# Optimization experiments

Hardware: AMD Instinct MI355X
Metric: run time of the kernel (lower is better)

Reference implementation:

```python
import jax, jax.numpy as jnp
import numpy as np

D_MODEL = 512
EPS = 1e-5  # torch LayerNorm default


def _layernorm(x, g, b):
    mu = jnp.mean(x, axis=-1, keepdims=True)
    var = jnp.mean(jnp.square(x - mu), axis=-1, keepdims=True)
    return (x - mu) * jax.lax.rsqrt(var + EPS) * g + b


def setup_inputs() -> dict:
    key = jax.random.key(0)
    ks = jax.random.split(key, 12)
    d = D_MODEL
    s = 1.0 / np.sqrt(d)
    s4 = 1.0 / np.sqrt(4 * d)
    return {
        "x": jax.random.normal(ks[0], (4, 4096, d), dtype=jnp.float32),
        "Wq": jax.random.uniform(ks[1], (d, d), jnp.float32, -s, s),
        "bq": jax.random.uniform(ks[2], (d,), jnp.float32, -s, s),
        "Wk": jax.random.uniform(ks[3], (d, d), jnp.float32, -s, s),
        "bk": jax.random.uniform(ks[4], (d,), jnp.float32, -s, s),
        "Wv": jax.random.uniform(ks[5], (d, d), jnp.float32, -s, s),
        "bv": jax.random.uniform(ks[6], (d,), jnp.float32, -s, s),
        "g1": jnp.ones((d,), jnp.float32),
        "b1": jnp.zeros((d,), jnp.float32),
        "g2": jnp.ones((d,), jnp.float32),
        "b2": jnp.zeros((d,), jnp.float32),
        "W1": jax.random.uniform(ks[7], (d, 4 * d), jnp.float32, -s, s),
        "bf1": jax.random.uniform(ks[8], (4 * d,), jnp.float32, -s, s),
        "W2": jax.random.uniform(ks[9], (4 * d, d), jnp.float32, -s4, s4),
        "bf2": jax.random.uniform(ks[10], (d,), jnp.float32, -s4, s4),
    }


def reference(x, Wq, bq, Wk, bk, Wv, bv, g1, b1, g2, b2, W1, bf1, W2, bf2):
    # QKV projections: [b, s, d]
    Q = jnp.einsum("bsd,de->bse", x, Wq) + bq
    K = jnp.einsum("bsd,de->bse", x, Wk) + bk
    V = jnp.einsum("bsd,de->bse", x, Wv) + bv
    scale = 1.0 / jnp.sqrt(jnp.float32(K.shape[-1]))
    scores = jnp.einsum("bqd,bkd->bqk", Q, K) * scale  # [b, s, s]
    attn = jax.nn.softmax(scores, axis=-1)
    att = jnp.einsum("bqk,bkd->bqd", attn, V)
    x = _layernorm(x + att, g1, b1)
    h = jax.nn.relu(jnp.einsum("bsd,df->bsf", x, W1) + bf1)
    ffn = jnp.einsum("bsf,fd->bsd", h, W2) + bf2
    return _layernorm(x + ffn, g2, b2)
```

## Files before the change

kernel.cpp:

```cpp
#include <hip/hip_runtime.h>
#include <hip/hip_bf16.h>

typedef unsigned short u16;
typedef short bf16x8 __attribute__((ext_vector_type(8)));
typedef float f32x4 __attribute__((ext_vector_type(4)));

__device__ __forceinline__ float b2f(u16 u) {
  union { float f; unsigned int i; } v; v.i = ((unsigned int)u) << 16; return v.f;
}
__device__ __forceinline__ u16 f2b(float f) {
  union { float f; unsigned int i; } v; v.f = f;
  unsigned int r = v.i + 0x7fffu + ((v.i >> 16) & 1u);
  return (u16)(r >> 16);
}
__device__ __forceinline__ u16 to_b(float v) { return f2b(v); }
__device__ __forceinline__ u16 to_b(u16 v) { return v; }

__device__ __forceinline__ void gl_lds16(const u16* g, u16* l) {
  __builtin_amdgcn_global_load_lds(
      (const __attribute__((address_space(1))) unsigned int*)g,
      (__attribute__((address_space(3))) unsigned int*)l, 16, 0, 0);
}

#define VMW4()  asm volatile("s_waitcnt vmcnt(4)" ::: "memory")
#define VMW0()  asm volatile("s_waitcnt vmcnt(0)" ::: "memory")
#define CFENCE() asm volatile("" ::: "memory")

template <bool RELU, bool ATOMIC>
__global__ __launch_bounds__(256)
void gemm_nt(const u16* __restrict__ A, const u16* __restrict__ Bt,
             const float* __restrict__ bias, void* __restrict__ Cv,
             int N, int K, int nsplit, int lda, int ldb, int ldc,
             long sA, long sB, long sC, float scale) {
  __shared__ __align__(16) u16 As[128 * 64];
  __shared__ __align__(16) u16 Bs[128 * 64];
  const int z = blockIdx.z;
  const int batch = z / nsplit, split = z - batch * nsplit;
  const int Ks = K / nsplit;
  const u16* Ab = A + (long)batch * sA + (long)split * Ks;
  const u16* Bb = Bt + (long)batch * sB + (long)split * Ks;
  const int f = blockIdx.x + gridDim.x * blockIdx.y;
  const int xcd = f & 7, idx = f >> 3;
  const int bx = idx % gridDim.x;
  const int by = xcd * (gridDim.y >> 3) + idx / gridDim.x;
  const int m0 = by * 128, n0 = bx * 128;
  const int t = threadIdx.x, w = t >> 6, lane = t & 63;
  const int wm = (w >> 1) * 64, wn = (w & 1) * 64;
  const int lr = lane & 15, q = lane >> 4;

  int srow[4], scol[4];
#pragma unroll
  for (int i = 0; i < 4; i++) {
    int n = w * 256 + i * 64 + lane;
    srow[i] = n >> 3;
    scol[i] = (((n & 7) ^ ((n >> 3) & 7)) * 8);
  }

  f32x4 acc[4][4];
#pragma unroll
  for (int i = 0; i < 4; i++)
#pragma unroll
    for (int j = 0; j < 4; j++) acc[i][j] = (f32x4){0.f, 0.f, 0.f, 0.f};

  for (int k0 = 0; k0 < Ks; k0 += 64) {
#pragma unroll
    for (int i = 0; i < 4; i++)
      gl_lds16(Ab + (long)(m0 + srow[i]) * lda + k0 + scol[i], &As[(w * 256 + i * 64) * 8]);
#pragma unroll
    for (int i = 0; i < 4; i++)
      gl_lds16(Bb + (long)(n0 + srow[i]) * ldb + k0 + scol[i], &Bs[(w * 256 + i * 64) * 8]);
    __syncthreads();
#pragma unroll
    for (int kk = 0; kk < 2; kk++) {
      bf16x8 af[4], bfr[4];
#pragma unroll
      for (int i = 0; i < 4; i++) {
        int row = wm + i * 16 + lr;
        af[i] = *(const bf16x8*)&As[row * 64 + (((kk * 4 + q) ^ (row & 7)) * 8)];
      }
#pragma unroll
      for (int j = 0; j < 4; j++) {
        int row = wn + j * 16 + lr;
        bfr[j] = *(const bf16x8*)&Bs[row * 64 + (((kk * 4 + q) ^ (row & 7)) * 8)];
      }
#pragma unroll
      for (int i = 0; i < 4; i++)
#pragma unroll
        for (int j = 0; j < 4; j++)
          acc[i][j] = __builtin_amdgcn_mfma_f32_16x16x32_bf16(af[i], bfr[j], acc[i][j], 0, 0, 0);
    }
    __syncthreads();
  }

#pragma unroll
  for (int j = 0; j < 4; j++) {
    int cg = n0 + wn + j * 16 + lr;
    float bb = (!ATOMIC && bias) ? bias[cg] : 0.0f;
#pragma unroll
    for (int i = 0; i < 4; i++) {
      int rbase = m0 + wm + i * 16 + q * 4;
#pragma unroll
      for (int r = 0; r < 4; r++) {
        float vv = acc[i][j][r] * scale;
        if (ATOMIC) {
          atomicAdd((float*)Cv + (long)batch * sC + (long)(rbase + r) * ldc + cg, vv);
        } else {
          vv += bb;
          if (RELU) vv = fmaxf(vv, 0.0f);
          ((u16*)Cv)[(long)batch * sC + (long)(rbase + r) * ldc + cg] = f2b(vv);
        }
      }
    }
  }
}

#define STAGE_K(kvv, kcc, sel)                                               \
  {                                                                          \
    _Pragma("unroll") for (int rr = 0; rr < 4; rr++)                         \
        gl_lds16(Kbase + (long)((kvv) * 128 + srow[rr]) * 1536 +             \
                     (kcc) * 128 + scol8[rr],                                \
                 &B2[(sel)][ldsd[rr]]);                                      \
  }
#define STAGE_V(kvv, dcc, sel)                                               \
  {                                                                          \
    _Pragma("unroll") for (int rr = 0; rr < 4; rr++)                         \
        gl_lds16(Vtb + (long)((dcc) * 128 + srow[rr]) * 4096 +               \
                     (kvv) * 128 + scol8[rr],                                \
                 &B2[(sel)][ldsd[rr]]);                                      \
  }

__global__ __launch_bounds__(512, 2)
void flash_attn(const u16* __restrict__ QKV, const u16* __restrict__ Vt,
                u16* __restrict__ attp, float* __restrict__ lbp, float scl) {
  __shared__ __align__(16) u16 B2[2][128 * 128];
  __shared__ __align__(16) u16 Pb[128 * 136];
  const int flat = blockIdx.x;
  const int batch = (flat & 7) >> 1, half = flat & 1, qt = flat >> 3;
  const int t = threadIdx.x, w = t >> 6, lane = t & 63;
  const int lr = lane & 15, q = lane >> 4;
  const long rowbase = (long)batch * 4096 + qt * 128;
  const u16* Qrow  = QKV + (rowbase + w * 16 + lr) * 1536;
  const u16* Kbase = QKV + ((long)batch * 4096 + half * 2048) * 1536 + 512;
  const u16* Vtb   = Vt + (long)batch * 512 * 4096 + half * 2048;
  u16* Pw = &Pb[w * (16 * 136)];

  int srow[4], scol8[4], ldsd[4];
#pragma unroll
  for (int rr = 0; rr < 4; rr++) {
    int n = rr * 512 + t;
    srow[rr] = n >> 4;
    scol8[rr] = ((n & 15) ^ ((n >> 4) & 15)) * 8;
    ldsd[rr] = (rr * 512 + w * 64) * 8;
  }

  f32x4 O[32];
#pragma unroll
  for (int i = 0; i < 32; i++) O[i] = (f32x4){0.f, 0.f, 0.f, 0.f};
  float lsum[4] = {0.f, 0.f, 0.f, 0.f};

  STAGE_K(0, 0, 0);
  int par = 0;

  for (int kv = 0; kv < 16; kv++) {
    f32x4 S[8];
#pragma unroll
    for (int j = 0; j < 8; j++) S[j] = (f32x4){0.f, 0.f, 0.f, 0.f};

#pragma unroll
    for (int kc = 0; kc < 4; kc++) {
      bf16x8 Qf[4];
#pragma unroll
      for (int ss = 0; ss < 4; ss++)
        Qf[ss] = *(const bf16x8*)(Qrow + kc * 128 + ss * 32 + q * 8);
      __builtin_amdgcn_sched_barrier(0);
      if (kc < 3) { STAGE_K(kv, kc + 1, par ^ 1); }
      else        { STAGE_V(kv, 0, par ^ 1); }
      VMW4();
      __builtin_amdgcn_s_barrier();
      CFENCE();
      __builtin_amdgcn_s_setprio(1);
#pragma unroll
      for (int ss = 0; ss < 4; ss++)
#pragma unroll
        for (int j = 0; j < 8; j++) {
          int row = j * 16 + lr;
          bf16x8 Kf = *(const bf16x8*)&B2[par][row * 128 + (((ss * 4 + q) ^ lr) * 8)];
          S[j] = __builtin_amdgcn_mfma_f32_16x16x32_bf16(Qf[ss], Kf, S[j], 0, 0, 0);
        }
      __builtin_amdgcn_s_setprio(0);
      CFENCE();
      __builtin_amdgcn_s_barrier();
      par ^= 1;
    }

    float psum[4] = {0.f, 0.f, 0.f, 0.f};
#pragma unroll
    for (int j = 0; j < 8; j++)
#pragma unroll
      for (int r = 0; r < 4; r++) {
        float e = __expf(S[j][r] * scl);
        psum[r] += e;
        Pw[(q * 4 + r) * 136 + j * 16 + lr] = f2b(e);
      }
#pragma unroll
    for (int r = 0; r < 4; r++) {
#pragma unroll
      for (int o = 1; o < 16; o <<= 1) psum[r] += __shfl_xor(psum[r], o);
      lsum[r] += psum[r];
    }
    bf16x8 Pf[4];
#pragma unroll
    for (int t4 = 0; t4 < 4; t4++)
      Pf[t4] = *(const bf16x8*)&Pw[lr * 136 + t4 * 32 + q * 8];

#pragma unroll
    for (int dc = 0; dc < 4; dc++) {
      if (dc < 3) {
        STAGE_V(kv, dc + 1, par ^ 1);
        VMW4();
      } else if (kv < 15) {
        STAGE_K(kv + 1, 0, par ^ 1);
        VMW4();
      } else {
        VMW0();
      }
      __builtin_amdgcn_s_barrier();
      CFENCE();
      __builtin_amdgcn_s_setprio(1);
#pragma unroll
      for (int t4 = 0; t4 < 4; t4++)
#pragma unroll
        for (int j = 0; j < 8; j++) {
          int row = j * 16 + lr;
          bf16x8 Vf = *(const bf16x8*)&B2[par][row * 128 + (((t4 * 4 + q) ^ lr) * 8)];
          O[dc * 8 + j] = __builtin_amdgcn_mfma_f32_16x16x32_bf16(Pf[t4], Vf, O[dc * 8 + j], 0, 0, 0);
        }
      __builtin_amdgcn_s_setprio(0);
      CFENCE();
      __builtin_amdgcn_s_barrier();
      par ^= 1;
    }
  }

  u16* op = attp + (long)half * 16384 * 512;
#pragma unroll
  for (int i = 0; i < 32; i++) {
    int col = (i >> 3) * 128 + (i & 7) * 16 + lr;
#pragma unroll
    for (int r = 0; r < 4; r++)
      op[(rowbase + w * 16 + q * 4 + r) * 512 + col] = f2b(O[i][r]);
  }
  if (lr == 0)
#pragma unroll
    for (int r = 0; r < 4; r++)
      lbp[(long)half * 16384 + rowbase + w * 16 + q * 4 + r] = lsum[r];
}

template <typename TS>
__global__ __launch_bounds__(1024)
void transpose_b(const TS* __restrict__ src, u16* __restrict__ dst,
                 int R, int Cc, int src_ld, long sbs, long dbs) {
  __shared__ u16 tile[32][33];
  int r = blockIdx.y * 32 + threadIdx.y;
  int c = blockIdx.x * 32 + threadIdx.x;
  tile[threadIdx.y][threadIdx.x] = to_b(src[(long)blockIdx.z * sbs + (long)r * src_ld + c]);
  __syncthreads();
  int rr = blockIdx.x * 32 + threadIdx.y;
  int cc = blockIdx.y * 32 + threadIdx.x;
  dst[(long)blockIdx.z * dbs + (long)rr * R + cc] = tile[threadIdx.x][threadIdx.y];
}

__global__ __launch_bounds__(1024)
void prep(const float* __restrict__ Wq, const float* __restrict__ Wk,
          const float* __restrict__ Wv, const float* __restrict__ W1,
          const float* __restrict__ W2, const float* __restrict__ bq,
          const float* __restrict__ bk, const float* __restrict__ bv,
          const float* __restrict__ x, u16* __restrict__ wqkvt,
          u16* __restrict__ w1t, u16* __restrict__ w2t,
          float* __restrict__ bqkv, u16* __restrict__ xb) {
  __shared__ u16 tile[32][33];
  const int b = blockIdx.x;
  const int t = threadIdx.x;
  const int tx = t & 31, ty = t >> 5;
  if (b < 768) {
    const int wsel = b >> 8, idx = b & 255;
    const int bx = idx & 15, by = idx >> 4;
    const float* src = wsel == 0 ? Wq : (wsel == 1 ? Wk : Wv);
    u16* dst = wqkvt + wsel * 512 * 512;
    tile[ty][tx] = f2b(src[(by * 32 + ty) * 512 + bx * 32 + tx]);
    __syncthreads();
    dst[(bx * 32 + ty) * 512 + by * 32 + tx] = tile[tx][ty];
  } else if (b < 1792) {
    const int idx = b - 768;
    const int bx = idx & 63, by = idx >> 6;
    tile[ty][tx] = f2b(W1[(by * 32 + ty) * 2048 + bx * 32 + tx]);
    __syncthreads();
    w1t[(bx * 32 + ty) * 512 + by * 32 + tx] = tile[tx][ty];
  } else if (b < 2816) {
    const int idx = b - 1792;
    const int bx = idx & 15, by = idx >> 4;
    tile[ty][tx] = f2b(W2[(by * 32 + ty) * 512 + bx * 32 + tx]);
    __syncthreads();
    w2t[(bx * 32 + ty) * 2048 + by * 32 + tx] = tile[tx][ty];
  } else if (b < 3840) {
    const long i = ((long)(b - 2816) * 1024 + t) * 8;
    float4 a0 = *(const float4*)(x + i);
    float4 a1 = *(const float4*)(x + i + 4);
    u16 tmp[8] = {f2b(a0.x), f2b(a0.y), f2b(a0.z), f2b(a0.w),
                  f2b(a1.x), f2b(a1.y), f2b(a1.z), f2b(a1.w)};
    *(uint4*)(xb + i) = *(uint4*)tmp;
  } else {
    const int i = (b - 3840) * 1024 + t;
    if (i < 512) bqkv[i] = bq[i];
    else if (i < 1024) bqkv[i] = bk[i - 512];
    else if (i < 1536) bqkv[i] = bv[i - 1024];
  }
}

__global__ __launch_bounds__(256)
void add_ln_att(const float* __restrict__ X, const u16* __restrict__ attp,
                const float* __restrict__ lbp,
                const float* __restrict__ g, const float* __restrict__ b,
                u16* __restrict__ O) {
  const int row = blockIdx.x * 4 + (threadIdx.x >> 6);
  const int lane = threadIdx.x & 63;
  const size_t base = (size_t)row * 512 + lane * 8;
  const float inv = 1.0f / (lbp[row] + lbp[16384 + row]);
  uint4 p0 = *(const uint4*)(attp + base);
  uint4 p1 = *(const uint4*)(attp + 16384L * 512 + base);
  const u16* s0 = (const u16*)&p0;
  const u16* s1 = (const u16*)&p1;
  float z[8];
  float s1a = 0.f, s2a = 0.f;
#pragma unroll
  for (int i = 0; i < 8; i++) {
    z[i] = X[base + i] + (b2f(s0[i]) + b2f(s1[i])) * inv;
    s1a += z[i]; s2a += z[i] * z[i];
  }
#pragma unroll
  for (int o = 32; o > 0; o >>= 1) { s1a += __shfl_xor(s1a, o); s2a += __shfl_xor(s2a, o); }
  const float mu = s1a * (1.0f / 512.0f);
  const float var = s2a * (1.0f / 512.0f) - mu * mu;
  const float rstd = rsqrtf(var + 1e-5f);
#pragma unroll
  for (int i = 0; i < 8; i++) {
    int c = lane * 8 + i;
    O[base + i] = f2b((z[i] - mu) * rstd * g[c] + b[c]);
  }
}

__global__ __launch_bounds__(256)
void add_ln_ffn(const u16* __restrict__ X, const u16* __restrict__ P0,
                const u16* __restrict__ P1, const float* __restrict__ eb,
                const float* __restrict__ g, const float* __restrict__ b,
                float* __restrict__ O) {
  const int row = blockIdx.x * 4 + (threadIdx.x >> 6);
  const int lane = threadIdx.x & 63;
  const size_t base = (size_t)row * 512 + lane * 8;
  uint4 xv = *(const uint4*)(X + base);
  uint4 a0 = *(const uint4*)(P0 + base);
  uint4 a1 = *(const uint4*)(P1 + base);
  const u16* xs = (const u16*)&xv;
  const u16* s0 = (const u16*)&a0;
  const u16* s1 = (const u16*)&a1;
  float z[8];
  float s1a = 0.f, s2a = 0.f;
#pragma unroll
  for (int i = 0; i < 8; i++) {
    int c = lane * 8 + i;
    z[i] = b2f(xs[i]) + b2f(s0[i]) + b2f(s1[i]) + eb[c];
    s1a += z[i]; s2a += z[i] * z[i];
  }
#pragma unroll
  for (int o = 32; o > 0; o >>= 1) { s1a += __shfl_xor(s1a, o); s2a += __shfl_xor(s2a, o); }
  const float mu = s1a * (1.0f / 512.0f);
  const float var = s2a * (1.0f / 512.0f) - mu * mu;
  const float rstd = rsqrtf(var + 1e-5f);
#pragma unroll
  for (int i = 0; i < 8; i++) {
    int c = lane * 8 + i;
    O[base + i] = (z[i] - mu) * rstd * g[c] + b[c];
  }
}

extern "C" void kernel_launch(void* const* d_in, const int* in_sizes, int n_in,
                              void* d_out, int out_size, void* d_ws, size_t ws_size,
                              hipStream_t stream) {
  const float* x   = (const float*)d_in[0];
  const float* Wq  = (const float*)d_in[1];
  const float* bq  = (const float*)d_in[2];
  const float* Wk  = (const float*)d_in[3];
  const float* bk  = (const float*)d_in[4];
  const float* Wv  = (const float*)d_in[5];
  const float* bv  = (const float*)d_in[6];
  const float* g1  = (const float*)d_in[7];
  const float* b1  = (const float*)d_in[8];
  const float* g2  = (const float*)d_in[9];
  const float* b2  = (const float*)d_in[10];
  const float* W1  = (const float*)d_in[11];
  const float* bf1 = (const float*)d_in[12];
  const float* W2  = (const float*)d_in[13];
  const float* bf2 = (const float*)d_in[14];
  float* out = (float*)d_out;

  char* ws = (char*)d_ws;
  const size_t MB = 1048576;
  u16*   QKV   = (u16*)(ws + 0);
  u16*   Vt    = (u16*)(ws + 48 * MB);
  u16*   attp  = (u16*)(ws + 64 * MB);
  u16*   h     = (u16*)(ws + 64 * MB);
  float* lbp   = (float*)(ws + 128 * MB);
  u16*   x1    = (u16*)(ws + 129 * MB);
  u16*   ffnp  = (u16*)(ws + 145 * MB);
  u16*   xb    = (u16*)(ws + 145 * MB);
  u16*   wqkvt = (u16*)(ws + 177 * MB);
  u16*   w1t   = wqkvt + 1536 * 512;
  u16*   w2t   = w1t + 2048 * 512;
  float* bqkv  = (float*)(w2t + 512 * 2048);

  prep<<<3842, 1024, 0, stream>>>(Wq, Wk, Wv, W1, W2, bq, bk, bv, x,
                                  wqkvt, w1t, w2t, bqkv, xb);

  gemm_nt<false, false><<<dim3(12, 128, 1), 256, 0, stream>>>(
      xb, wqkvt, bqkv, QKV, 1536, 512, 1, 512, 512, 1536, 0, 0, 0, 1.0f);

  transpose_b<u16><<<dim3(16, 128, 4), dim3(32, 32), 0, stream>>>(
      QKV + 1024, Vt, 4096, 512, 1536, 4096L * 1536, 512L * 4096);

  const float scl = 0.044194173824159216f;
  flash_attn<<<dim3(256, 1, 1), 512, 0, stream>>>(QKV, Vt, attp, lbp, scl);

  add_ln_att<<<4096, 256, 0, stream>>>(x, attp, lbp, g1, b1, x1);
  gemm_nt<true, false><<<dim3(16, 128, 1), 256, 0, stream>>>(
      x1, w1t, bf1, h, 2048, 512, 1, 512, 512, 2048, 0, 0, 0, 1.0f);
  gemm_nt<false, false><<<dim3(4, 128, 2), 256, 0, stream>>>(
      h, w2t, nullptr, ffnp, 512, 1024, 1, 2048, 2048, 512,
      1024, 1024, 16384L * 512, 1.0f);
  add_ln_ffn<<<4096, 256, 0, stream>>>(
      x1, ffnp, ffnp + 16384L * 512, bf2, g2, b2, out);
}
```

Baseline: 490.2 us.

## Enlarge GEMM tiles to 256x256 with 512 threads and double-buffered LDS prefetch

The bf16 NT GEMM now uses 256x256 output tiles computed by 8 waves (each 128x64), instead of 128x128 tiles with 4 waves. The LDS staging buffers are double-buffered: the next K-slice is issued with global_load_lds before computing the current one, with a vmcnt wait and raw s_barrier replacing __syncthreads. The aim is more operand reuse per byte loaded and overlap of global loads with MFMA work. In exchange, each block uses about 128KB of LDS and 128 accumulator registers per thread, which limits it to one block per CU, and the grids shrink (384, 512 and 256 blocks), so wave balance across CUs may suffer.

New measurement: 520.5 us. 1.06x slower.

```diff
diff --git a/kernel.cpp b/kernel.cpp
--- a/kernel.cpp
+++ b/kernel.cpp
@@ -22,18 +22,29 @@
       (__attribute__((address_space(3))) unsigned int*)l, 16, 0, 0);
 }
 
+#define VMW8()  asm volatile("s_waitcnt vmcnt(8)" ::: "memory")
 #define VMW4()  asm volatile("s_waitcnt vmcnt(4)" ::: "memory")
 #define VMW0()  asm volatile("s_waitcnt vmcnt(0)" ::: "memory")
 #define CFENCE() asm volatile("" ::: "memory")
 
+#define G2STAGE(k0v, sel)                                                    \
+  {                                                                          \
+    _Pragma("unroll") for (int i = 0; i < 4; i++)                            \
+        gl_lds16(Ab + (long)(m0 + srow[i]) * lda + (k0v) + scol[i],          \
+                 &As[sel][ldsd[i]]);                                         \
+    _Pragma("unroll") for (int i = 0; i < 4; i++)                            \
+        gl_lds16(Bb + (long)(n0 + srow[i]) * ldb + (k0v) + scol[i],          \
+                 &Bs[sel][ldsd[i]]);                                         \
+  }
+
 template <bool RELU, bool ATOMIC>
-__global__ __launch_bounds__(256)
+__global__ __launch_bounds__(512, 2)
 void gemm_nt(const u16* __restrict__ A, const u16* __restrict__ Bt,
              const float* __restrict__ bias, void* __restrict__ Cv,
              int N, int K, int nsplit, int lda, int ldb, int ldc,
              long sA, long sB, long sC, float scale) {
-  __shared__ __align__(16) u16 As[128 * 64];
-  __shared__ __align__(16) u16 Bs[128 * 64];
+  __shared__ __align__(16) u16 As[2][256 * 64];
+  __shared__ __align__(16) u16 Bs[2][256 * 64];
   const int z = blockIdx.z;
   const int batch = z / nsplit, split = z - batch * nsplit;
   const int Ks = K / nsplit;
@@ -43,53 +54,61 @@
   const int xcd = f & 7, idx = f >> 3;
   const int bx = idx % gridDim.x;
   const int by = xcd * (gridDim.y >> 3) + idx / gridDim.x;
-  const int m0 = by * 128, n0 = bx * 128;
+  const int m0 = by * 256, n0 = bx * 256;
   const int t = threadIdx.x, w = t >> 6, lane = t & 63;
-  const int wm = (w >> 1) * 64, wn = (w & 1) * 64;
+  const int wm = (w >> 2) * 128, wn = (w & 3) * 64;
   const int lr = lane & 15, q = lane >> 4;
 
-  int srow[4], scol[4];
+  int srow[4], scol[4], ldsd[4];
 #pragma unroll
   for (int i = 0; i < 4; i++) {
-    int n = w * 256 + i * 64 + lane;
+    int n = i * 512 + t;
     srow[i] = n >> 3;
     scol[i] = (((n & 7) ^ ((n >> 3) & 7)) * 8);
-  }
-
-  f32x4 acc[4][4];
-#pragma unroll
-  for (int i = 0; i < 4; i++)
+    ldsd[i] = (i * 512 + w * 64) * 8;
+  }
+
+  f32x4 acc[8][4];
+#pragma unroll
+  for (int i = 0; i < 8; i++)
 #pragma unroll
     for (int j = 0; j < 4; j++) acc[i][j] = (f32x4){0.f, 0.f, 0.f, 0.f};
 
-  for (int k0 = 0; k0 < Ks; k0 += 64) {
-#pragma unroll
-    for (int i = 0; i < 4; i++)
-      gl_lds16(Ab + (long)(m0 + srow[i]) * lda + k0 + scol[i], &As[(w * 256 + i * 64) * 8]);
-#pragma unroll
-    for (int i = 0; i < 4; i++)
-      gl_lds16(Bb + (long)(n0 + srow[i]) * ldb + k0 + scol[i], &Bs[(w * 256 + i * 64) * 8]);
-    __syncthreads();
+  const int nk = Ks >> 6;
+  G2STAGE(0, 0);
+  int pb = 0;
+
+  for (int ks = 0; ks < nk; ks++) {
+    if (ks + 1 < nk) {
+      G2STAGE((ks + 1) << 6, pb ^ 1);
+      VMW8();
+    } else {
+      VMW0();
+    }
+    __builtin_amdgcn_s_barrier();
+    CFENCE();
 #pragma unroll
     for (int kk = 0; kk < 2; kk++) {
-      bf16x8 af[4], bfr[4];
-#pragma unroll
-      for (int i = 0; i < 4; i++) {
+      bf16x8 af[8], bfr[4];
+#pragma unroll
+      for (int i = 0; i < 8; i++) {
         int row = wm + i * 16 + lr;
-        af[i] = *(const bf16x8*)&As[row * 64 + (((kk * 4 + q) ^ (row & 7)) * 8)];
+        af[i] = *(const bf16x8*)&As[pb][row * 64 + (((kk * 4 + q) ^ (row & 7)) * 8)];
       }
 #pragma unroll
       for (int j = 0; j < 4; j++) {
         int row = wn + j * 16 + lr;
-        bfr[j] = *(const bf16x8*)&Bs[row * 64 + (((kk * 4 + q) ^ (row & 7)) * 8)];
+        bfr[j] = *(const bf16x8*)&Bs[pb][row * 64 + (((kk * 4 + q) ^ (row & 7)) * 8)];
       }
 #pragma unroll
-      for (int i = 0; i < 4; i++)
+      for (int i = 0; i < 8; i++)
 #pragma unroll
         for (int j = 0; j < 4; j++)
           acc[i][j] = __builtin_amdgcn_mfma_f32_16x16x32_bf16(af[i], bfr[j], acc[i][j], 0, 0, 0);
     }
-    __syncthreads();
+    CFENCE();
+    __builtin_amdgcn_s_barrier();
+    pb ^= 1;
   }
 
 #pragma unroll
@@ -97,7 +116,7 @@
     int cg = n0 + wn + j * 16 + lr;
     float bb = (!ATOMIC && bias) ? bias[cg] : 0.0f;
 #pragma unroll
-    for (int i = 0; i < 4; i++) {
+    for (int i = 0; i < 8; i++) {
       int rbase = m0 + wm + i * 16 + q * 4;
 #pragma unroll
       for (int r = 0; r < 4; r++) {
@@ -421,7 +440,7 @@
   prep<<<3842, 1024, 0, stream>>>(Wq, Wk, Wv, W1, W2, bq, bk, bv, x,
                                   wqkvt, w1t, w2t, bqkv, xb);
 
-  gemm_nt<false, false><<<dim3(12, 128, 1), 256, 0, stream>>>(
+  gemm_nt<false, false><<<dim3(6, 64, 1), 512, 0, stream>>>(
       xb, wqkvt, bqkv, QKV, 1536, 512, 1, 512, 512, 1536, 0, 0, 0, 1.0f);
 
   transpose_b<u16><<<dim3(16, 128, 4), dim3(32, 32), 0, stream>>>(
@@ -431,9 +450,9 @@
   flash_attn<<<dim3(256, 1, 1), 512, 0, stream>>>(QKV, Vt, attp, lbp, scl);
 
   add_ln_att<<<4096, 256, 0, stream>>>(x, attp, lbp, g1, b1, x1);
-  gemm_nt<true, false><<<dim3(16, 128, 1), 256, 0, stream>>>(
+  gemm_nt<true, false><<<dim3(8, 64, 1), 512, 0, stream>>>(
       x1, w1t, bf1, h, 2048, 512, 1, 512, 512, 2048, 0, 0, 0, 1.0f);
-  gemm_nt<false, false><<<dim3(4, 128, 2), 256, 0, stream>>>(
+  gemm_nt<false, false><<<dim3(2, 64, 2), 512, 0, stream>>>(
       h, w2t, nullptr, ffnp, 512, 1024, 1, 2048, 2048, 512,
       1024, 1024, 16384L * 512, 1.0f);
   add_ln_ffn<<<4096, 256, 0, stream>>>(
```
